# Performance work log

Measured on AMD Instinct MI355X. Metric: run time of the kernel, lower is better.

Reference implementation:

```python
import jax, jax.numpy as jnp
import numpy as np

N = 32000   # nodes
E = 256000  # edges
G = 64      # graphs
IN = 64     # input feature dim
TD = 32     # time embedding dim
D = 128     # hidden dim
HEADS = 4
C = D // HEADS  # per-head channels = 32
ED = 16     # edge feature dim
L = 4       # num SBlocks
FF = 4 * D  # MLP hidden


def _ln(x, g, b):
    m = x.mean(-1, keepdims=True)
    v = ((x - m) ** 2).mean(-1, keepdims=True)
    return (x - m) / jnp.sqrt(v + 1e-5) * g + b


def _time_enc(t):
    half = TD // 2
    fac = jnp.exp(jnp.arange(half, dtype=jnp.float32) * (-jnp.log(10000.0) / (half - 1 + 1e-8)))
    ang = t.astype(jnp.float32)[:, None] * fac[None, :]
    return jnp.concatenate([jnp.sin(ang), jnp.cos(ang)], axis=-1)


def setup_inputs() -> dict:
    key = jax.random.key(0)
    ks = iter(jax.random.split(key, 64))
    nrm = lambda shape: jax.random.normal(next(ks), shape, dtype=jnp.float32) * 0.02
    x = jax.random.normal(next(ks), (N, IN), dtype=jnp.float32)
    t = jax.random.randint(next(ks), (N,), 0, 128, dtype=jnp.int32)
    edge_index = jax.random.randint(next(ks), (2, E), 0, N, dtype=jnp.int32)
    edge_attr = jax.random.normal(next(ks), (E, ED), dtype=jnp.float32)
    batch = jnp.sort(jax.random.randint(next(ks), (N,), 0, G, dtype=jnp.int32))
    p = {
        'Win': nrm((IN + TD, D)), 'b_in': jnp.zeros((D,), jnp.float32),
        'Wq': nrm((L, D, D)), 'bq': jnp.zeros((L, D), jnp.float32),
        'Wk': nrm((L, D, D)), 'bk': jnp.zeros((L, D), jnp.float32),
        'Wv': nrm((L, D, D)), 'bv': jnp.zeros((L, D), jnp.float32),
        'We': nrm((L, ED, D)), 'be': jnp.zeros((L, D), jnp.float32),
        'Wskip': nrm((L, D, D)), 'bskip': jnp.zeros((L, D), jnp.float32),
        'Wbeta': nrm((L, 3 * D)),
        'ln1_g': jnp.ones((L, D), jnp.float32), 'ln1_b': jnp.zeros((L, D), jnp.float32),
        'Wff1': nrm((L, D, FF)), 'bff1': jnp.zeros((L, FF), jnp.float32),
        'Wff2': nrm((L, FF, D)), 'bff2': jnp.zeros((L, D), jnp.float32),
        'ln2_g': jnp.ones((L, D), jnp.float32), 'ln2_b': jnp.zeros((L, D), jnp.float32),
        'Wh1': nrm((2 * D, D)), 'bh1': jnp.zeros((D,), jnp.float32),
        'Wh2': nrm((D, 2)), 'bh2': jnp.zeros((2,), jnp.float32),
    }
    return {'x': x, 't': t, 'edge_index': edge_index, 'edge_attr': edge_attr, 'batch': batch, **p}


def reference(x, t, edge_index, edge_attr, batch, Win, b_in, Wq, bq, Wk, bk, Wv, bv, We, be,
              Wskip, bskip, Wbeta, ln1_g, ln1_b, Wff1, bff1, Wff2, bff2, ln2_g, ln2_b,
              Wh1, bh1, Wh2, bh2):
    # input projection with sinusoidal time encoding
    h = jnp.concatenate([x, _time_enc(t)], axis=-1)
    h = jax.nn.relu(h @ Win + b_in)
    src, dst = edge_index[0], edge_index[1]
    for i in range(L):
        # TransformerConv (multi-head, edge_attr fused into key & value, beta skip)
        q = (h @ Wq[i] + bq[i]).reshape(N, HEADS, C)
        k = (h @ Wk[i] + bk[i]).reshape(N, HEADS, C)
        v = (h @ Wv[i] + bv[i]).reshape(N, HEADS, C)
        e = (edge_attr @ We[i] + be[i]).reshape(E, HEADS, C)
        kj = k[src] + e                     # [E,H,C] gather
        vj = v[src] + e
        alpha = (q[dst] * kj).sum(-1) / jnp.sqrt(jnp.asarray(C, h.dtype))  # [E,H]
        amax = jax.ops.segment_max(alpha, dst, num_segments=N)
        ex = jnp.exp(alpha - amax[dst])
        den = jax.ops.segment_sum(ex, dst, num_segments=N)
        w = ex / den[dst]                   # segment softmax over incoming edges
        out = jax.ops.segment_sum(vj * w[..., None], dst, num_segments=N).reshape(N, D)
        xr = h @ Wskip[i] + bskip[i]
        beta = jax.nn.sigmoid(jnp.concatenate([out, xr, out - xr], -1) @ Wbeta[i])[:, None]
        xs = beta * xr + (1.0 - beta) * out
        h = _ln(h + xs, ln1_g[i], ln1_b[i])
        ff = jax.nn.relu(h @ Wff1[i] + bff1[i]) @ Wff2[i] + bff2[i]
        h = _ln(h + ff, ln2_g[i], ln2_b[i])
    # last-timestep masked readout
    tf = t.astype(h.dtype)
    tmax = jax.ops.segment_max(tf, batch, num_segments=G)
    m = tf == tmax[batch]
    mf = m.astype(h.dtype)[:, None]
    cnt = jax.ops.segment_sum(mf, batch, num_segments=G)
    gmean = jax.ops.segment_sum(h * mf, batch, num_segments=G) / jnp.maximum(cnt, 1.0)
    gmax = jax.ops.segment_max(jnp.where(m[:, None], h, -1e30), batch, num_segments=G)
    g = jnp.concatenate([gmean, gmax], axis=-1)
    return jax.nn.relu(g @ Wh1 + bh1) @ Wh2 + bh2
```

## Files before the change

### kernel.cpp

```cpp
#include <hip/hip_runtime.h>

#define N_NODES 32000
#define N_EDGES 256000
#define N_GRAPH 64
#define NLAYER  4

typedef __attribute__((ext_vector_type(8))) short short8;
typedef __attribute__((ext_vector_type(4))) float f32x4;

__device__ __forceinline__ float bf2f(unsigned short u){
  return __uint_as_float(((unsigned int)u) << 16);
}
__device__ __forceinline__ unsigned short f2bf(float f){
  unsigned int x = __float_as_uint(f);
  x = x + 0x7fffu + ((x >> 16) & 1u);
  return (unsigned short)(x >> 16);
}
__device__ __forceinline__ float ldf(const void* p, int i, int isbf){
  if(isbf) return bf2f(((const unsigned short*)p)[i]);
  return ((const float*)p)[i];
}

__global__ void TactileGAT_43207370997900_kernel() {}

__global__ void sentinel_kernel(unsigned short* out){
  int i = blockIdx.x * 64 + threadIdx.x;
  if(i < 2 * N_GRAPH) out[i] = (unsigned short)0x4000;
}

__global__ void detect_kernel(const unsigned int* ones_words, int* flag){
  if(blockIdx.x == 0 && threadIdx.x == 0)
    flag[0] = (ones_words[0] == 0x3F800000u) ? 0 : 1;
}

__global__ void zero_kernel(int* p, int n){
  int i = blockIdx.x * 256 + threadIdx.x;
  if(i < n) p[i] = 0;
}

__global__ void deg_kernel(const int* dst, int* deg){
  int e = blockIdx.x * 256 + threadIdx.x;
  if(e < N_EDGES) atomicAdd(&deg[dst[e]], 1);
}

__global__ void blocksum_kernel(const int* deg, int* psum){
  __shared__ int s[256];
  int b = blockIdx.x, tid = threadIdx.x;
  int i = b * 256 + tid;
  s[tid] = (i < N_NODES) ? deg[i] : 0;
  __syncthreads();
  for(int off = 128; off > 0; off = off / 2){
    if(tid < off) s[tid] = s[tid] + s[tid + off];
    __syncthreads();
  }
  if(tid == 0) psum[b] = s[0];
}

__global__ void scanp_kernel(int* psum){
  __shared__ int s[128];
  int tid = threadIdx.x;
  int v = (tid < 125) ? psum[tid] : 0;
  s[tid] = v;
  __syncthreads();
  for(int off = 1; off < 128; off = off * 2){
    int tv = (tid >= off) ? s[tid - off] : 0;
    __syncthreads();
    s[tid] = s[tid] + tv;
    __syncthreads();
  }
  if(tid < 125) psum[tid] = s[tid] - v;
}

__global__ void rowptr_kernel(const int* deg, const int* psum, int* rowptr,
                              int* cursor){
  __shared__ int s[256];
  int b = blockIdx.x, tid = threadIdx.x;
  int i = b * 256 + tid;
  int v = (i < N_NODES) ? deg[i] : 0;
  s[tid] = v;
  __syncthreads();
  for(int off = 1; off < 256; off = off * 2){
    int tv = (tid >= off) ? s[tid - off] : 0;
    __syncthreads();
    s[tid] = s[tid] + tv;
    __syncthreads();
  }
  int excl = s[tid] - v + psum[b];
  if(i < N_NODES){ rowptr[i] = excl; cursor[i] = excl; }
  if(i == N_NODES - 1) rowptr[N_NODES] = excl + v;
}

__global__ void scatter_kernel(const int* dst, const int* src, int* cursor,
                               int* csr_e, int* csr_s){
  int e = blockIdx.x * 256 + threadIdx.x;
  if(e < N_EDGES){
    int pos = atomicAdd(&cursor[dst[e]], 1);
    csr_e[pos] = e;
    csr_s[pos] = src[e];
  }
}

__global__ void eap_kernel(const void* ea, const int* csr_e, const int* flag,
                           unsigned short* eap){
  int idx = blockIdx.x * 256 + threadIdx.x;
  if(idx >= N_EDGES * 32) return;
  int slot = idx >> 5, j = idx & 31;
  float v = (j < 16) ? ldf(ea, csr_e[slot] * 16 + j, flag[0]) : 0.f;
  eap[idx] = f2bf(v);
}

__global__ void wep_kernel(const void* We, const int* flag, unsigned short* WeP){
  int idx = blockIdx.x * 256 + threadIdx.x;
  if(idx >= NLAYER * 128 * 32) return;
  int i = idx >> 12, rem = idx & 4095, n = rem >> 5, k = rem & 31;
  float v = (k < 16) ? ldf(We, i * 2048 + k * 128 + n, flag[0]) : 0.f;
  WeP[idx] = f2bf(v);
}

__global__ void pack_kernel(const void* Wq, const void* Wk, const void* Wv,
                            const void* Wsk, const void* Wff1, const void* Wff2,
                            const int* flag, unsigned short* WTq,
                            unsigned short* WT1, unsigned short* WT2){
  int idx = blockIdx.x * 256 + threadIdx.x;
  int isbf = flag[0];
  int i = idx / 196608;
  if(i >= NLAYER) return;
  int rem = idx - i * 196608;
  int seg = rem / 65536;
  int off = rem - seg * 65536;
  if(seg == 0){
    int n = off >> 7, k = off & 127;
    int sel = n >> 7, c = n & 127;
    const void* W = (sel == 0) ? Wq : (sel == 1) ? Wk : (sel == 2) ? Wv : Wsk;
    WTq[i * 65536 + off] = f2bf(ldf(W, i * 16384 + k * 128 + c, isbf));
  } else if(seg == 1){
    int n = off >> 7, k = off & 127;
    WT1[i * 65536 + off] = f2bf(ldf(Wff1, i * 65536 + k * 512 + n, isbf));
  } else {
    int n = off >> 9, k = off & 511;
    WT2[i * 65536 + off] = f2bf(ldf(Wff2, i * 65536 + k * 128 + n, isbf));
  }
}

__global__ void xprep_kernel(const void* x, const int* t, const int* flag,
                             unsigned short* xin){
  int idx = blockIdx.x * 256 + threadIdx.x;
  if(idx >= N_NODES * 128) return;
  int n = idx >> 7, c = idx & 127;
  float v;
  if(c < 64){
    v = ldf(x, n * 64 + c, flag[0]);
  } else if(c < 96){
    int j  = c - 64;
    int jj = (j < 16) ? j : (j - 16);
    float fac = expf((float)jj * (-9.210340371976184f / 15.00000001f));
    float ang = (float)t[n] * fac;
    v = (j < 16) ? sinf(ang) : cosf(ang);
  } else {
    v = 0.f;
  }
  xin[idx] = f2bf(v);
}

__global__ void winp_kernel(const void* Win, const int* flag,
                            unsigned short* WTin){
  int idx = blockIdx.x * 256 + threadIdx.x;
  if(idx >= 128 * 128) return;
  int c = idx >> 7, k = idx & 127;
  float v = (k < 96) ? ldf(Win, k * 128 + c, flag[0]) : 0.f;
  WTin[idx] = f2bf(v);
}

__global__ void gemm_frag(const unsigned short* A, const unsigned short* WT,
                          const void* bias, int boff, const int* flag,
                          int K, int nbx, void* Y, int obf, int ystride,
                          int act){
  int tid = threadIdx.x;
  int bx = blockIdx.x % nbx;
  int by = blockIdx.x / nbx;
  int m0 = by * 128, c0 = bx * 128;
  int wv = tid / 64, lane = tid % 64;
  int q = lane / 16, r = lane % 16;
  const unsigned short* Ap0 = A + (m0 + wv * 32 + r) * K + q * 8;
  const unsigned short* Ap1 = Ap0 + 16 * K;
  const unsigned short* Wp = WT + (c0 + r) * K + q * 8;
  f32x4 acc[2][8];
  for(int g = 0; g < 2; g++)
    for(int tt = 0; tt < 8; tt++)
      for(int i = 0; i < 4; i++) acc[g][tt][i] = 0.f;
  for(int k0 = 0; k0 < K; k0 += 32){
    short8 a0 = *(const short8*)(Ap0 + k0);
    short8 a1 = *(const short8*)(Ap1 + k0);
    for(int tt = 0; tt < 8; tt++){
      short8 b8 = *(const short8*)(Wp + tt * 16 * K + k0);
      acc[0][tt] = __builtin_amdgcn_mfma_f32_16x16x32_bf16(a0, b8, acc[0][tt], 0, 0, 0);
      acc[1][tt] = __builtin_amdgcn_mfma_f32_16x16x32_bf16(a1, b8, acc[1][tt], 0, 0, 0);
    }
  }
  int isbf = flag[0];
  for(int tt = 0; tt < 8; tt++){
    int c = c0 + tt * 16 + r;
    float bv = ldf(bias, boff + c, isbf);
    for(int g = 0; g < 2; g++){
      for(int i = 0; i < 4; i++){
        int row = m0 + wv * 32 + g * 16 + q * 4 + i;
        float v = acc[g][tt][i] + bv;
        if(act == 1) v = fmaxf(v, 0.f);
        if(obf) ((unsigned short*)Y)[row * ystride + c] = f2bf(v);
        else    ((float*)Y)[row * ystride + c] = v;
      }
    }
  }
}

__global__ void edp_frag(const unsigned short* A, const unsigned short* WT,
                         const void* be, int boff, const int* flag,
                         unsigned int* edl){
  int tid = threadIdx.x;
  int m0 = blockIdx.x * 128;
  int wv = tid / 64, lane = tid % 64;
  int q = lane / 16, r = lane % 16;
  const unsigned short* Ap0 = A + (m0 + wv * 32 + r) * 32 + q * 8;
  const unsigned short* Ap1 = Ap0 + 16 * 32;
  const unsigned short* Wp = WT + r * 32 + q * 8;
  f32x4 acc[2][8];
  for(int g = 0; g < 2; g++)
    for(int tt = 0; tt < 8; tt++)
      for(int i = 0; i < 4; i++) acc[g][tt][i] = 0.f;
  short8 a0 = *(const short8*)(Ap0);
  short8 a1 = *(const short8*)(Ap1);
  for(int tt = 0; tt < 8; tt++){
    short8 b8 = *(const short8*)(Wp + tt * 16 * 32);
    acc[0][tt] = __builtin_amdgcn_mfma_f32_16x16x32_bf16(a0, b8, acc[0][tt], 0, 0, 0);
    acc[1][tt] = __builtin_amdgcn_mfma_f32_16x16x32_bf16(a1, b8, acc[1][tt], 0, 0, 0);
  }
  int isbf = flag[0];
  for(int tt = 0; tt < 4; tt++){
    int cc0 = tt * 16 + r;
    float bv0 = ldf(be, boff + cc0, isbf);
    float bv1 = ldf(be, boff + cc0 + 64, isbf);
    for(int g = 0; g < 2; g++){
      for(int i = 0; i < 4; i++){
        int row = m0 + wv * 32 + g * 16 + q * 4 + i;
        unsigned int w = (unsigned int)f2bf(acc[g][tt][i] + bv0)
                       | ((unsigned int)f2bf(acc[g][tt + 4][i] + bv1) << 16);
        edl[(size_t)row * 64 + cc0] = w;
      }
    }
  }
}

__global__ void qkvs_frag(const unsigned short* A, const unsigned short* WTq,
                          const void* b0, const void* b1, const void* b2,
                          const void* b3, int boff, const int* flag,
                          float* qs, unsigned int* kvp){
  int tid = threadIdx.x;
  int sel = blockIdx.x % 4;
  int by  = blockIdx.x / 4;
  int m0 = by * 128;
  int wv = tid / 64, lane = tid % 64;
  int q = lane / 16, r = lane % 16;
  const unsigned short* Ap0 = A + (m0 + wv * 32 + r) * 128 + q * 8;
  const unsigned short* Ap1 = Ap0 + 16 * 128;
  const unsigned short* Wp = WTq + (sel * 128 + r) * 128 + q * 8;
  f32x4 acc[2][8];
  for(int g = 0; g < 2; g++)
    for(int tt = 0; tt < 8; tt++)
      for(int i = 0; i < 4; i++) acc[g][tt][i] = 0.f;
  for(int k0 = 0; k0 < 128; k0 += 32){
    short8 a0 = *(const short8*)(Ap0 + k0);
    short8 a1 = *(const short8*)(Ap1 + k0);
    for(int tt = 0; tt < 8; tt++){
      short8 b8 = *(const short8*)(Wp + tt * 16 * 128 + k0);
      acc[0][tt] = __builtin_amdgcn_mfma_f32_16x16x32_bf16(a0, b8, acc[0][tt], 0, 0, 0);
      acc[1][tt] = __builtin_amdgcn_mfma_f32_16x16x32_bf16(a1, b8, acc[1][tt], 0, 0, 0);
    }
  }
  int isbf = flag[0];
  const void* B = (sel == 0) ? b0 : (sel == 1) ? b1 : (sel == 2) ? b2 : b3;
  if(sel == 0 || sel == 3){
    for(int tt = 0; tt < 8; tt++){
      int cc = tt * 16 + r;
      float bv = ldf(B, boff + cc, isbf);
      for(int g = 0; g < 2; g++){
        for(int i = 0; i < 4; i++){
          int row = m0 + wv * 32 + g * 16 + q * 4 + i;
          float v = acc[g][tt][i] + bv;
          if(sel == 0) qs[row * 256 + cc] = v;
          else         qs[row * 256 + 128 + cc] = v;
        }
      }
    }
  } else {
    int voff = sel - 1;
    for(int tt = 0; tt < 4; tt++){
      int cc0 = tt * 16 + r;
      float bv0 = ldf(B, boff + cc0, isbf);
      float bv1 = ldf(B, boff + cc0 + 64, isbf);
      for(int g = 0; g < 2; g++){
        for(int i = 0; i < 4; i++){
          int row = m0 + wv * 32 + g * 16 + q * 4 + i;
          unsigned int w = (unsigned int)f2bf(acc[g][tt][i] + bv0)
                         | ((unsigned int)f2bf(acc[g][tt + 4][i] + bv1) << 16);
          kvp[row * 128 + 2 * cc0 + voff] = w;
        }
      }
    }
  }
}

#define CH 4
#define ASLICE (CH * 144 + 16)

__device__ __forceinline__ void attn_epilogue(
    int n, int L, float o0, float o1,
    const float* __restrict__ qs, const unsigned short* __restrict__ h,
    const void* Wbeta, int wboff, const void* lng, int lgoff,
    const void* lnb, int lboff, int isbf, unsigned short* __restrict__ h2){
  float xr0 = qs[n * 256 + 128 + L];
  float xr1 = qs[n * 256 + 192 + L];
  float hv0 = bf2f(h[n * 128 + L]);
  float hv1 = bf2f(h[n * 128 + 64 + L]);
  float part = o0 * ldf(Wbeta, wboff + L, isbf)
             + xr0 * ldf(Wbeta, wboff + 128 + L, isbf)
             + (o0 - xr0) * ldf(Wbeta, wboff + 256 + L, isbf)
             + o1 * ldf(Wbeta, wboff + 64 + L, isbf)
             + xr1 * ldf(Wbeta, wboff + 192 + L, isbf)
             + (o1 - xr1) * ldf(Wbeta, wboff + 320 + L, isbf);
#pragma unroll
  for(int mk = 1; mk < 64; mk <<= 1) part += __shfl_xor(part, mk, 64);
  float beta = 1.f / (1.f + __expf(-part));
  float y0 = hv0 + beta * xr0 + (1.f - beta) * o0;
  float y1 = hv1 + beta * xr1 + (1.f - beta) * o1;
  float s = y0 + y1;
#pragma unroll
  for(int mk = 1; mk < 64; mk <<= 1) s += __shfl_xor(s, mk, 64);
  float mean = s * (1.f / 128.f);
  float dy0 = y0 - mean, dy1 = y1 - mean;
  float v2 = dy0 * dy0 + dy1 * dy1;
#pragma unroll
  for(int mk = 1; mk < 64; mk <<= 1) v2 += __shfl_xor(v2, mk, 64);
  float inv = 1.f / sqrtf(v2 * (1.f / 128.f) + 1e-5f);
  h2[n * 128 + L]      = f2bf(dy0 * inv * ldf(lng, lgoff + L, isbf)
                              + ldf(lnb, lboff + L, isbf));
  h2[n * 128 + 64 + L] = f2bf(dy1 * inv * ldf(lng, lgoff + 64 + L, isbf)
                              + ldf(lnb, lboff + 64 + L, isbf));
}

__global__ __launch_bounds__(256, 8)
void attn_epi1_kernel(const float* __restrict__ qs,
                      const unsigned int* __restrict__ kvp,
                      const unsigned int* __restrict__ edl,
                      const int* __restrict__ csr_s,
                      const int* __restrict__ rowptr,
                      const void* __restrict__ Wbeta, int wboff,
                      const void* __restrict__ lng, int lgoff,
                      const void* __restrict__ lnb, int lboff,
                      const unsigned short* __restrict__ h,
                      const int* __restrict__ flag,
                      unsigned short* __restrict__ h2){
  __shared__ float lds[4 * ASLICE];
  int wv = threadIdx.x >> 6, L = threadIdx.x & 63;
  float* sprod  = lds + wv * ASLICE;
  float* salpha = sprod + CH * 144;
  int n = blockIdx.x * 4 + wv;
  int isbf = flag[0];
  int hL = L >> 5, c31 = L & 31;
  float q0 = qs[n * 256 + L]      * 0.17677669529663687f;
  float q1 = qs[n * 256 + 64 + L] * 0.17677669529663687f;
  int beg = rowptr[n], end = rowptr[n + 1];
  float m0 = -1e30f, l0 = 0.f, a0s = 0.f;
  float m1 = -1e30f, l1 = 0.f, a1s = 0.f;
  for(int ci = beg; ci < end; ci += CH){
    int Ep = end - ci; if(Ep > CH) Ep = CH;
    uint2 kw[CH]; unsigned int ew[CH];
#pragma unroll
    for(int i = 0; i < CH; i++){
      kw[i] = make_uint2(0u, 0u); ew[i] = 0u;
      if(i < Ep){
        int s = __builtin_amdgcn_readfirstlane(csr_s[ci + i]);
        kw[i] = *(const uint2*)(kvp + (size_t)s * 128 + 2 * L);
        ew[i] = edl[(size_t)(ci + i) * 64 + L];
      }
    }
    float vd0[CH], vd1[CH];
#pragma unroll
    for(int i = 0; i < CH; i++){
      float e0 = bf2f((unsigned short)(ew[i] & 0xffffu));
      float e1 = bf2f((unsigned short)(ew[i] >> 16));
      float kd0 = bf2f((unsigned short)(kw[i].x & 0xffffu)) + e0;
      float kd1 = bf2f((unsigned short)(kw[i].x >> 16)) + e1;
      vd0[i] = bf2f((unsigned short)(kw[i].y & 0xffffu)) + e0;
      vd1[i] = bf2f((unsigned short)(kw[i].y >> 16)) + e1;
      sprod[i * 144 + hL * 36 + c31]       = q0 * kd0;
      sprod[i * 144 + (2 + hL) * 36 + c31] = q1 * kd1;
    }
    asm volatile("" ::: "memory");
    {
      int i2 = L >> 4, h4 = (L >> 2) & 3, sub = L & 3;
      const f32x4* pp = (const f32x4*)(sprod + i2 * 144 + h4 * 36 + sub * 8);
      f32x4 va = pp[0], vb = pp[1];
      float sv = (va[0] + va[1]) + (va[2] + va[3])
               + ((vb[0] + vb[1]) + (vb[2] + vb[3]));
      sv += __shfl_xor(sv, 1, 64);
      sv += __shfl_xor(sv, 2, 64);
      if(sub == 0) salpha[i2 * 4 + h4] = sv;
    }
    asm volatile("" ::: "memory");
#pragma unroll
    for(int i = 0; i < CH; i++){
      if(i < Ep){
        float p0 = salpha[i * 4 + hL];
        float p1 = salpha[i * 4 + 2 + hL];
        float mn0 = fmaxf(m0, p0), mn1 = fmaxf(m1, p1);
        float g0 = __expf(fminf(p0, m0) - mn0);
        float g1 = __expf(fminf(p1, m1) - mn1);
        float pp0 = (p0 <= m0) ? g0 : 1.f, sc0 = (p0 <= m0) ? 1.f : g0;
        float pp1 = (p1 <= m1) ? g1 : 1.f, sc1 = (p1 <= m1) ? 1.f : g1;
        l0 = l0 * sc0 + pp0;  a0s = a0s * sc0 + pp0 * vd0[i];  m0 = mn0;
        l1 = l1 * sc1 + pp1;  a1s = a1s * sc1 + pp1 * vd1[i];  m1 = mn1;
      }
    }
    asm volatile("" ::: "memory");
  }
  float o0 = (l0 > 0.f) ? a0s / l0 : 0.f;
  float o1 = (l1 > 0.f) ? a1s / l1 : 0.f;
  attn_epilogue(n, L, o0, o1, qs, h, Wbeta, wboff, lng, lgoff, lnb, lboff,
                isbf, h2);
}

__global__ __launch_bounds__(256, 4)
void attn_epi1_inl(const float* __restrict__ qs,
                   const unsigned int* __restrict__ kvp,
                   const unsigned short* __restrict__ eap,
                   const unsigned short* __restrict__ WeP, int lay,
                   const void* __restrict__ be, int beoff,
                   const int* __restrict__ csr_s,
                   const int* __restrict__ rowptr,
                   const void* __restrict__ Wbeta, int wboff,
                   const void* __restrict__ lng, int lgoff,
                   const void* __restrict__ lnb, int lboff,
                   const unsigned short* __restrict__ h,
                   const int* __restrict__ flag,
                   unsigned short* __restrict__ h2){
  __shared__ float lds[4 * ASLICE];
  int wv = threadIdx.x >> 6, L = threadIdx.x & 63;
  float* sprod  = lds + wv * ASLICE;
  float* salpha = sprod + CH * 144;
  int n = blockIdx.x * 4 + wv;
  int isbf = flag[0];
  int hL = L >> 5, c31 = L & 31;
  float wec0[16], wec1[16];
  {
    const short8* wp = (const short8*)(WeP + (size_t)lay * 4096 + L * 32);
    short8 wa = wp[0], wb = wp[1];
    const short8* wq = (const short8*)(WeP + (size_t)lay * 4096 + (L + 64) * 32);
    short8 wc = wq[0], wd = wq[1];
#pragma unroll
    for(int j = 0; j < 8; j++){
      wec0[j]     = bf2f((unsigned short)wa[j]);
      wec0[8 + j] = bf2f((unsigned short)wb[j]);
      wec1[j]     = bf2f((unsigned short)wc[j]);
      wec1[8 + j] = bf2f((unsigned short)wd[j]);
    }
  }
  float be0 = ldf(be, beoff + L, isbf);
  float be1 = ldf(be, beoff + 64 + L, isbf);
  float q0 = qs[n * 256 + L]      * 0.17677669529663687f;
  float q1 = qs[n * 256 + 64 + L] * 0.17677669529663687f;
  int beg = rowptr[n], end = rowptr[n + 1];
  float m0 = -1e30f, l0 = 0.f, a0s = 0.f;
  float m1 = -1e30f, l1 = 0.f, a1s = 0.f;
  for(int ci = beg; ci < end; ci += CH){
    int Ep = end - ci; if(Ep > CH) Ep = CH;
    uint2 kw[CH]; short8 ea_a[CH], ea_b[CH];
#pragma unroll
    for(int i = 0; i < CH; i++){
      kw[i] = make_uint2(0u, 0u);
      ea_a[i] = (short8)0; ea_b[i] = (short8)0;
      if(i < Ep){
        int s = __builtin_amdgcn_readfirstlane(csr_s[ci + i]);
        kw[i] = *(const uint2*)(kvp + (size_t)s * 128 + 2 * L);
        const short8* er = (const short8*)(eap + (size_t)(ci + i) * 32);
        ea_a[i] = er[0]; ea_b[i] = er[1];
      }
    }
    float vd0[CH], vd1[CH];
#pragma unroll
    for(int i = 0; i < CH; i++){
      float ed0 = be0, ed1 = be1;
#pragma unroll
      for(int j = 0; j < 8; j++){
        float va = bf2f((unsigned short)ea_a[i][j]);
        float vb = bf2f((unsigned short)ea_b[i][j]);
        ed0 += va * wec0[j] + vb * wec0[8 + j];
        ed1 += va * wec1[j] + vb * wec1[8 + j];
      }
      float kd0 = bf2f((unsigned short)(kw[i].x & 0xffffu)) + ed0;
      float kd1 = bf2f((unsigned short)(kw[i].x >> 16)) + ed1;
      vd0[i] = bf2f((unsigned short)(kw[i].y & 0xffffu)) + ed0;
      vd1[i] = bf2f((unsigned short)(kw[i].y >> 16)) + ed1;
      sprod[i * 144 + hL * 36 + c31]       = q0 * kd0;
      sprod[i * 144 + (2 + hL) * 36 + c31] = q1 * kd1;
    }
    asm volatile("" ::: "memory");
    {
      int i2 = L >> 4, h4 = (L >> 2) & 3, sub = L & 3;
      const f32x4* pp = (const f32x4*)(sprod + i2 * 144 + h4 * 36 + sub * 8);
      f32x4 va = pp[0], vb = pp[1];
      float sv = (va[0] + va[1]) + (va[2] + va[3])
               + ((vb[0] + vb[1]) + (vb[2] + vb[3]));
      sv += __shfl_xor(sv, 1, 64);
      sv += __shfl_xor(sv, 2, 64);
      if(sub == 0) salpha[i2 * 4 + h4] = sv;
    }
    asm volatile("" ::: "memory");
#pragma unroll
    for(int i = 0; i < CH; i++){
      if(i < Ep){
        float p0 = salpha[i * 4 + hL];
        float p1 = salpha[i * 4 + 2 + hL];
        float mn0 = fmaxf(m0, p0), mn1 = fmaxf(m1, p1);
        float g0 = __expf(fminf(p0, m0) - mn0);
        float g1 = __expf(fminf(p1, m1) - mn1);
        float pp0 = (p0 <= m0) ? g0 : 1.f, sc0 = (p0 <= m0) ? 1.f : g0;
        float pp1 = (p1 <= m1) ? g1 : 1.f, sc1 = (p1 <= m1) ? 1.f : g1;
        l0 = l0 * sc0 + pp0;  a0s = a0s * sc0 + pp0 * vd0[i];  m0 = mn0;
        l1 = l1 * sc1 + pp1;  a1s = a1s * sc1 + pp1 * vd1[i];  m1 = mn1;
      }
    }
    asm volatile("" ::: "memory");
  }
  float o0 = (l0 > 0.f) ? a0s / l0 : 0.f;
  float o1 = (l1 > 0.f) ? a1s / l1 : 0.f;
  attn_epilogue(n, L, o0, o1, qs, h, Wbeta, wboff, lng, lgoff, lnb, lboff,
                isbf, h2);
}

__global__ void ff2_ln_kernel(const unsigned short* A, const unsigned short* WT,
                              const void* bias, int boff,
                              const unsigned short* h2,
                              const void* lng, int lgoff,
                              const void* lnb, int lboff,
                              const int* flag, unsigned short* outh){
  __shared__ float Ys[64 * 133];
  __shared__ float smean[64];
  __shared__ float sinv[64];
  int tid = threadIdx.x;
  int m0 = blockIdx.x * 64;
  int wv = tid / 64, lane = tid % 64;
  int q = lane / 16, r = lane % 16;
  const unsigned short* Ap = A + (m0 + wv * 16 + r) * 512 + q * 8;
  const unsigned short* Wp = WT + r * 512 + q * 8;
  f32x4 acc[8];
  for(int tt = 0; tt < 8; tt++)
    for(int i = 0; i < 4; i++) acc[tt][i] = 0.f;
  for(int k0 = 0; k0 < 512; k0 += 32){
    short8 a8 = *(const short8*)(Ap + k0);
    for(int tt = 0; tt < 8; tt++){
      short8 b8 = *(const short8*)(Wp + tt * 16 * 512 + k0);
      acc[tt] = __builtin_amdgcn_mfma_f32_16x16x32_bf16(a8, b8, acc[tt], 0, 0, 0);
    }
  }
  int isbf = flag[0];
  for(int tt = 0; tt < 8; tt++){
    int c = tt * 16 + r;
    float bv = ldf(bias, boff + c, isbf);
    for(int i = 0; i < 4; i++){
      int rl = wv * 16 + q * 4 + i;
      float v = acc[tt][i] + bv;
      Ys[rl * 133 + c] = bf2f(h2[(m0 + rl) * 128 + c]) + v;
    }
  }
  __syncthreads();
  if(tid < 64){
    float s = 0.f, s2 = 0.f;
    for(int c = 0; c < 128; c++){
      float y = Ys[tid * 133 + c];
      s += y; s2 += y * y;
    }
    float mean = s * (1.f / 128.f);
    float var  = s2 * (1.f / 128.f) - mean * mean;
    smean[tid] = mean;
    sinv[tid]  = 1.f / sqrtf(var + 1e-5f);
  }
  __syncthreads();
  for(int tt = 0; tt < 8; tt++){
    int c = tt * 16 + r;
    float g = ldf(lng, lgoff + c, isbf);
    float b = ldf(lnb, lboff + c, isbf);
    for(int i = 0; i < 4; i++){
      int rl = wv * 16 + q * 4 + i;
      float y = Ys[rl * 133 + c];
      outh[(m0 + rl) * 128 + c] = f2bf((y - smean[rl]) * sinv[rl] * g + b);
    }
  }
}

__global__ void bounds_kernel(const int* batch, int* gstart, int* gend){
  int n = blockIdx.x * 256 + threadIdx.x;
  if(n >= N_NODES) return;
  int b = batch[n];
  if(n == 0 || batch[n - 1] != b) gstart[b] = n;
  if(n == N_NODES - 1 || batch[n + 1] != b) gend[b] = n + 1;
}

__global__ void readout_kernel(const int* t, const unsigned short* h,
                               const int* gstart, const int* gend, float* gbuf){
  __shared__ int redi[128];
  int g = blockIdx.x, d = threadIdx.x;
  int s = gstart[g], e = gend[g];
  int tm = -2147483647;
  for(int nn = s + d; nn < e; nn += 128){
    int tv = t[nn];
    tm = (tv > tm) ? tv : tm;
  }
  redi[d] = tm;
  __syncthreads();
  for(int off = 64; off > 0; off = off / 2){
    if(d < off) redi[d] = (redi[d + off] > redi[d]) ? redi[d + off] : redi[d];
    __syncthreads();
  }
  tm = redi[0];
  float sum = 0.f, mx = -1e30f;
  int cnt = 0;
  for(int nn = s; nn < e; nn++){
    if(t[nn] == tm){
      float hv = bf2f(h[nn * 128 + d]);
      sum += hv;
      mx = fmaxf(mx, hv);
      cnt = cnt + 1;
    }
  }
  gbuf[g * 256 + d]       = sum / (float)((cnt < 1) ? 1 : cnt);
  gbuf[g * 256 + 128 + d] = mx;
}

__global__ void mlp_kernel(const float* gbuf, const void* Wh1, const void* bh1,
                           const void* Wh2, const void* bh2, const int* flag,
                           void* outp){
  __shared__ float gs[256];
  __shared__ float r1[128];
  int g = blockIdx.x, d = threadIdx.x;
  int isbf = flag[0];
  gs[d]       = gbuf[g * 256 + d];
  gs[d + 128] = gbuf[g * 256 + 128 + d];
  __syncthreads();
  float acc = ldf(bh1, d, isbf);
  for(int k = 0; k < 256; k++) acc += gs[k] * ldf(Wh1, k * 128 + d, isbf);
  r1[d] = fmaxf(acc, 0.f);
  __syncthreads();
  if(d < 2){
    float a = ldf(bh2, d, isbf);
    for(int k = 0; k < 128; k++) a += r1[k] * ldf(Wh2, k * 2 + d, isbf);
    if(isbf) ((unsigned short*)outp)[g * 2 + d] = f2bf(a);
    else     ((float*)outp)[g * 2 + d] = a;
  }
}

extern "C" void kernel_launch(void* const* d_in, const int* in_sizes, int n_in,
                              void* d_out, int out_size, void* d_ws, size_t ws_size,
                              hipStream_t stream){
  const void* x          = d_in[0];
  const int*  t          = (const int*)d_in[1];
  const int*  edge_index = (const int*)d_in[2];
  const void* edge_attr  = d_in[3];
  const int*  batch      = (const int*)d_in[4];
  const void* Win  = d_in[5];  const void* b_in = d_in[6];
  const void* Wq   = d_in[7];  const void* bq   = d_in[8];
  const void* Wk   = d_in[9];  const void* bk   = d_in[10];
  const void* Wv   = d_in[11]; const void* bv   = d_in[12];
  const void* We   = d_in[13]; const void* be   = d_in[14];
  const void* Wsk  = d_in[15]; const void* bsk  = d_in[16];
  const void* Wbeta= d_in[17];
  const void* ln1g = d_in[18]; const void* ln1b = d_in[19];
  const void* Wff1 = d_in[20]; const void* bff1 = d_in[21];
  const void* Wff2 = d_in[22]; const void* bff2 = d_in[23];
  const void* ln2g = d_in[24]; const void* ln2b = d_in[25];
  const void* Wh1  = d_in[26]; const void* bh1  = d_in[27];
  const void* Wh2  = d_in[28]; const void* bh2  = d_in[29];
  (void)in_sizes; (void)n_in; (void)out_size;

  char* p = (char*)d_ws;
  unsigned short* h    = (unsigned short*)p; p += (long long)N_NODES * 128 * 2;
  unsigned short* h2   = (unsigned short*)p; p += (long long)N_NODES * 128 * 2;
  float* qs            = (float*)p;          p += (long long)N_NODES * 256 * 4;
  unsigned int* kvp    = (unsigned int*)p;   p += (long long)N_NODES * 128 * 4;
  unsigned short* ffmid= (unsigned short*)p; p += (long long)N_NODES * 512 * 2;
  unsigned short* WTq  = (unsigned short*)p; p += (long long)NLAYER * 65536 * 2;
  unsigned short* WT1  = (unsigned short*)p; p += (long long)NLAYER * 65536 * 2;
  unsigned short* WT2  = (unsigned short*)p; p += (long long)NLAYER * 65536 * 2;
  float* gbuf = (float*)p; p += (long long)N_GRAPH * 256 * 4;
  int* flag   = (int*)p;   p += 4;
  int* rowptr = (int*)p;   p += (long long)(N_NODES + 1) * 4;
  int* cursor = (int*)p;   p += (long long)N_NODES * 4;
  int* deg    = (int*)p;   p += (long long)N_NODES * 4;
  int* gstart = (int*)p;   p += (long long)N_GRAPH * 4;
  int* gend   = (int*)p;   p += (long long)N_GRAPH * 4;
  int* psum   = (int*)p;   p += 128 * 4;
  int* csr_e  = (int*)p;   p += (long long)N_EDGES * 4;
  int* csr_s  = (int*)p;   p += (long long)N_EDGES * 4;
  unsigned short* eap = (unsigned short*)p; p += (long long)N_EDGES * 32 * 2;
  unsigned short* WeP = (unsigned short*)p; p += (long long)NLAYER * 128 * 32 * 2;
  unsigned short* WTin= (unsigned short*)p; p += (long long)128 * 128 * 2;
  unsigned int* edl   = (unsigned int*)p;
  size_t need_edl = (size_t)((char*)edl - (char*)d_ws) + (size_t)N_EDGES * 64 * 4;
  int use_edl = (ws_size >= need_edl) ? 1 : 0;

  unsigned short* xin = ffmid;

  const int* esrc = edge_index;
  const int* edst = edge_index + N_EDGES;

  sentinel_kernel<<<2, 64, 0, stream>>>((unsigned short*)d_out);
  detect_kernel<<<1, 64, 0, stream>>>((const unsigned int*)ln1g, flag);

  int n_zero = N_NODES + 2 * N_GRAPH;
  zero_kernel<<<(n_zero + 255) / 256, 256, 0, stream>>>(deg, n_zero);

  pack_kernel<<<(NLAYER * 196608 + 255) / 256, 256, 0, stream>>>(
      Wq, Wk, Wv, Wsk, Wff1, Wff2, flag, WTq, WT1, WT2);
  deg_kernel<<<N_EDGES / 256, 256, 0, stream>>>(edst, deg);
  blocksum_kernel<<<125, 256, 0, stream>>>(deg, psum);
  scanp_kernel<<<1, 128, 0, stream>>>(psum);
  rowptr_kernel<<<125, 256, 0, stream>>>(deg, psum, rowptr, cursor);
  scatter_kernel<<<N_EDGES / 256, 256, 0, stream>>>(edst, esrc, cursor,
                                                    csr_e, csr_s);
  eap_kernel<<<(N_EDGES * 32) / 256, 256, 0, stream>>>(edge_attr, csr_e, flag, eap);
  wep_kernel<<<(NLAYER * 128 * 32) / 256, 256, 0, stream>>>(We, flag, WeP);

  xprep_kernel<<<(N_NODES * 128) / 256, 256, 0, stream>>>(x, t, flag, xin);
  winp_kernel<<<(128 * 128) / 256, 256, 0, stream>>>(Win, flag, WTin);
  gemm_frag<<<N_NODES / 128, 256, 0, stream>>>(
      xin, WTin, b_in, 0, flag, 128, 1, h, 1, 128, 1);

  int nby = N_NODES / 128;
  for(int i = 0; i < NLAYER; i++){
    if(use_edl)
      edp_frag<<<N_EDGES / 128, 256, 0, stream>>>(
          eap, WeP + (size_t)i * 4096, be, i * 128, flag, edl);
    qkvs_frag<<<4 * nby, 256, 0, stream>>>(
        h, WTq + (long long)i * 65536, bq, bk, bv, bsk, i * 128, flag, qs, kvp);
    if(use_edl)
      attn_epi1_kernel<<<N_NODES / 4, 256, 0, stream>>>(
          qs, kvp, edl, csr_s, rowptr, Wbeta, i * 384,
          ln1g, i * 128, ln1b, i * 128, h, flag, h2);
    else
      attn_epi1_inl<<<N_NODES / 4, 256, 0, stream>>>(
          qs, kvp, eap, WeP, i, be, i * 128, csr_s, rowptr, Wbeta, i * 384,
          ln1g, i * 128, ln1b, i * 128, h, flag, h2);
    gemm_frag<<<4 * nby, 256, 0, stream>>>(
        h2, WT1 + (long long)i * 65536, bff1, i * 512, flag, 128, 4,
        ffmid, 1, 512, 1);
    ff2_ln_kernel<<<N_NODES / 64, 256, 0, stream>>>(
        ffmid, WT2 + (long long)i * 65536, bff2, i * 128, h2,
        ln2g, i * 128, ln2b, i * 128, flag, h);
  }

  bounds_kernel<<<N_NODES / 256, 256, 0, stream>>>(batch, gstart, gend);
  readout_kernel<<<N_GRAPH, 128, 0, stream>>>(t, h, gstart, gend, gbuf);
  mlp_kernel<<<N_GRAPH, 128, 0, stream>>>(gbuf, Wh1, bh1, Wh2, bh2, flag, d_out);
}
```

Measured before the change: 991.3 us.

## Fuse FF1 and FF2+LayerNorm via LDS; widen attention edge chunk to 8

Merges the FF1 GEMM (with ReLU) and the FF2 GEMM + residual + LayerNorm into one kernel. The 512-wide intermediate for 32 rows stays in LDS as bf16, so the global ffmid round trip and one launch per layer go away. Separately, the edge-chunk size in the edl attention kernel goes from 4 to 8 with lower occupancy bounds, giving more loads in flight per chunk. Costs are extra LDS per block (about 33KB) and possibly fewer resident waves, and FF1 weights are reloaded for every 32-row tile.

New measurement: 922.0 us. -7.0%, faster.

```diff
diff --git a/kernel.cpp b/kernel.cpp
--- a/kernel.cpp
+++ b/kernel.cpp
@@ -309,8 +309,8 @@
   }
 }
 
-#define CH 4
-#define ASLICE (CH * 144 + 16)
+#define CH 8
+#define ASLICE (CH * 144 + CH * 4)
 
 __device__ __forceinline__ void attn_epilogue(
     int n, int L, float o0, float o1,
@@ -347,7 +347,7 @@
                               + ldf(lnb, lboff + 64 + L, isbf));
 }
 
-__global__ __launch_bounds__(256, 8)
+__global__ __launch_bounds__(256, 6)
 void attn_epi1_kernel(const float* __restrict__ qs,
                       const unsigned int* __restrict__ kvp,
                       const unsigned int* __restrict__ edl,
@@ -397,14 +397,18 @@
     }
     asm volatile("" ::: "memory");
     {
-      int i2 = L >> 4, h4 = (L >> 2) & 3, sub = L & 3;
-      const f32x4* pp = (const f32x4*)(sprod + i2 * 144 + h4 * 36 + sub * 8);
-      f32x4 va = pp[0], vb = pp[1];
-      float sv = (va[0] + va[1]) + (va[2] + va[3])
-               + ((vb[0] + vb[1]) + (vb[2] + vb[3]));
-      sv += __shfl_xor(sv, 1, 64);
-      sv += __shfl_xor(sv, 2, 64);
-      if(sub == 0) salpha[i2 * 4 + h4] = sv;
+      int i2b = L >> 4, h4 = (L >> 2) & 3, sub = L & 3;
+#pragma unroll
+      for(int half = 0; half < CH / 4; half++){
+        int i2 = i2b + half * 4;
+        const f32x4* pp = (const f32x4*)(sprod + i2 * 144 + h4 * 36 + sub * 8);
+        f32x4 va = pp[0], vb = pp[1];
+        float sv = (va[0] + va[1]) + (va[2] + va[3])
+                 + ((vb[0] + vb[1]) + (vb[2] + vb[3]));
+        sv += __shfl_xor(sv, 1, 64);
+        sv += __shfl_xor(sv, 2, 64);
+        if(sub == 0) salpha[i2 * 4 + h4] = sv;
+      }
     }
     asm volatile("" ::: "memory");
 #pragma unroll
@@ -429,6 +433,8 @@
                 isbf, h2);
 }
 
+#define CH4 4
+#define ASLICE4 (CH4 * 144 + CH4 * 4)
 __global__ __launch_bounds__(256, 4)
 void attn_epi1_inl(const float* __restrict__ qs,
                    const unsigned int* __restrict__ kvp,
@@ -443,10 +449,10 @@
                    const unsigned short* __restrict__ h,
                    const int* __restrict__ flag,
                    unsigned short* __restrict__ h2){
-  __shared__ float lds[4 * ASLICE];
+  __shared__ float lds[4 * ASLICE4];
   int wv = threadIdx.x >> 6, L = threadIdx.x & 63;
-  float* sprod  = lds + wv * ASLICE;
-  float* salpha = sprod + CH * 144;
+  float* sprod  = lds + wv * ASLICE4;
+  float* salpha = sprod + CH4 * 144;
   int n = blockIdx.x * 4 + wv;
   int isbf = flag[0];
   int hL = L >> 5, c31 = L & 31;
@@ -471,11 +477,11 @@
   int beg = rowptr[n], end = rowptr[n + 1];
   float m0 = -1e30f, l0 = 0.f, a0s = 0.f;
   float m1 = -1e30f, l1 = 0.f, a1s = 0.f;
-  for(int ci = beg; ci < end; ci += CH){
-    int Ep = end - ci; if(Ep > CH) Ep = CH;
-    uint2 kw[CH]; short8 ea_a[CH], ea_b[CH];
-#pragma unroll
-    for(int i = 0; i < CH; i++){
+  for(int ci = beg; ci < end; ci += CH4){
+    int Ep = end - ci; if(Ep > CH4) Ep = CH4;
+    uint2 kw[CH4]; short8 ea_a[CH4], ea_b[CH4];
+#pragma unroll
+    for(int i = 0; i < CH4; i++){
       kw[i] = make_uint2(0u, 0u);
       ea_a[i] = (short8)0; ea_b[i] = (short8)0;
       if(i < Ep){
@@ -485,9 +491,9 @@
         ea_a[i] = er[0]; ea_b[i] = er[1];
       }
     }
-    float vd0[CH], vd1[CH];
-#pragma unroll
-    for(int i = 0; i < CH; i++){
+    float vd0[CH4], vd1[CH4];
+#pragma unroll
+    for(int i = 0; i < CH4; i++){
       float ed0 = be0, ed1 = be1;
 #pragma unroll
       for(int j = 0; j < 8; j++){
@@ -516,7 +522,7 @@
     }
     asm volatile("" ::: "memory");
 #pragma unroll
-    for(int i = 0; i < CH; i++){
+    for(int i = 0; i < CH4; i++){
       if(i < Ep){
         float p0 = salpha[i * 4 + hL];
         float p1 = salpha[i * 4 + 2 + hL];
@@ -537,63 +543,108 @@
                 isbf, h2);
 }
 
-__global__ void ff2_ln_kernel(const unsigned short* A, const unsigned short* WT,
-                              const void* bias, int boff,
-                              const unsigned short* h2,
-                              const void* lng, int lgoff,
-                              const void* lnb, int lboff,
-                              const int* flag, unsigned short* outh){
-  __shared__ float Ys[64 * 133];
-  __shared__ float smean[64];
-  __shared__ float sinv[64];
+__global__ __launch_bounds__(256, 4)
+void ff_fused_kernel(const unsigned short* __restrict__ A,
+                     const unsigned short* __restrict__ WT1,
+                     const unsigned short* __restrict__ WT2,
+                     const void* __restrict__ b1, int b1off,
+                     const void* __restrict__ b2, int b2off,
+                     const void* __restrict__ lng, int lgoff,
+                     const void* __restrict__ lnb, int lboff,
+                     const int* __restrict__ flag,
+                     unsigned short* __restrict__ outh){
+  __shared__ __align__(16) float smemf[32 * 520 / 2];
+  __shared__ float smean[32], sinv[32];
+  unsigned short* mid = (unsigned short*)smemf;
+  float* Ys = smemf;
   int tid = threadIdx.x;
-  int m0 = blockIdx.x * 64;
-  int wv = tid / 64, lane = tid % 64;
-  int q = lane / 16, r = lane % 16;
-  const unsigned short* Ap = A + (m0 + wv * 16 + r) * 512 + q * 8;
-  const unsigned short* Wp = WT + r * 512 + q * 8;
-  f32x4 acc[8];
-  for(int tt = 0; tt < 8; tt++)
-    for(int i = 0; i < 4; i++) acc[tt][i] = 0.f;
-  for(int k0 = 0; k0 < 512; k0 += 32){
-    short8 a8 = *(const short8*)(Ap + k0);
+  int m0 = blockIdx.x * 32;
+  int wv = tid >> 6, lane = tid & 63;
+  int q = lane >> 4, r = lane & 15;
+  int isbf = flag[0];
+  {
+    const unsigned short* Ap0 = A + (m0 + r) * 128 + q * 8;
+    const unsigned short* Ap1 = Ap0 + 16 * 128;
+    const unsigned short* Wp = WT1 + (wv * 128 + r) * 128 + q * 8;
+    f32x4 acc[2][8];
+    for(int g = 0; g < 2; g++)
+      for(int tt = 0; tt < 8; tt++)
+        for(int i = 0; i < 4; i++) acc[g][tt][i] = 0.f;
+    for(int k0 = 0; k0 < 128; k0 += 32){
+      short8 a0 = *(const short8*)(Ap0 + k0);
+      short8 a1 = *(const short8*)(Ap1 + k0);
+      for(int tt = 0; tt < 8; tt++){
+        short8 b8 = *(const short8*)(Wp + tt * 16 * 128 + k0);
+        acc[0][tt] = __builtin_amdgcn_mfma_f32_16x16x32_bf16(a0, b8, acc[0][tt], 0, 0, 0);
+        acc[1][tt] = __builtin_amdgcn_mfma_f32_16x16x32_bf16(a1, b8, acc[1][tt], 0, 0, 0);
+      }
+    }
     for(int tt = 0; tt < 8; tt++){
-      short8 b8 = *(const short8*)(Wp + tt * 16 * 512 + k0);
-      acc[tt] = __builtin_amdgcn_mfma_f32_16x16x32_bf16(a8, b8, acc[tt], 0, 0, 0);
-    }
-  }
-  int isbf = flag[0];
-  for(int tt = 0; tt < 8; tt++){
-    int c = tt * 16 + r;
-    float bv = ldf(bias, boff + c, isbf);
-    for(int i = 0; i < 4; i++){
-      int rl = wv * 16 + q * 4 + i;
-      float v = acc[tt][i] + bv;
-      Ys[rl * 133 + c] = bf2f(h2[(m0 + rl) * 128 + c]) + v;
-    }
-  }
-  __syncthreads();
-  if(tid < 64){
+      int c = wv * 128 + tt * 16 + r;
+      float bv = ldf(b1, b1off + c, isbf);
+      for(int g = 0; g < 2; g++){
+        for(int i = 0; i < 4; i++){
+          int row = g * 16 + q * 4 + i;
+          mid[row * 520 + c] = f2bf(fmaxf(acc[g][tt][i] + bv, 0.f));
+        }
+      }
+    }
+  }
+  __syncthreads();
+  f32x4 acc2[2][2];
+  for(int g = 0; g < 2; g++)
+    for(int tt = 0; tt < 2; tt++)
+      for(int i = 0; i < 4; i++) acc2[g][tt][i] = 0.f;
+  {
+    const unsigned short* Wp2 = WT2 + (wv * 32 + r) * 512 + q * 8;
+    for(int k0 = 0; k0 < 512; k0 += 32){
+      short8 a0 = *(const short8*)(mid + r * 520 + k0 + q * 8);
+      short8 a1 = *(const short8*)(mid + (r + 16) * 520 + k0 + q * 8);
+      for(int tt = 0; tt < 2; tt++){
+        short8 b8 = *(const short8*)(Wp2 + tt * 16 * 512 + k0);
+        acc2[0][tt] = __builtin_amdgcn_mfma_f32_16x16x32_bf16(a0, b8, acc2[0][tt], 0, 0, 0);
+        acc2[1][tt] = __builtin_amdgcn_mfma_f32_16x16x32_bf16(a1, b8, acc2[1][tt], 0, 0, 0);
+      }
+    }
+  }
+  __syncthreads();
+  for(int tt = 0; tt < 2; tt++){
+    int c = wv * 32 + tt * 16 + r;
+    float bv = ldf(b2, b2off + c, isbf);
+    for(int g = 0; g < 2; g++){
+      for(int i = 0; i < 4; i++){
+        int row = g * 16 + q * 4 + i;
+        Ys[row * 132 + c] = bf2f(A[(m0 + row) * 128 + c]) + acc2[g][tt][i] + bv;
+      }
+    }
+  }
+  __syncthreads();
+  {
+    int row = tid >> 3, sub = tid & 7;
     float s = 0.f, s2 = 0.f;
-    for(int c = 0; c < 128; c++){
-      float y = Ys[tid * 133 + c];
+    for(int j = 0; j < 16; j++){
+      float y = Ys[row * 132 + sub * 16 + j];
       s += y; s2 += y * y;
     }
-    float mean = s * (1.f / 128.f);
-    float var  = s2 * (1.f / 128.f) - mean * mean;
-    smean[tid] = mean;
-    sinv[tid]  = 1.f / sqrtf(var + 1e-5f);
-  }
-  __syncthreads();
-  for(int tt = 0; tt < 8; tt++){
-    int c = tt * 16 + r;
-    float g = ldf(lng, lgoff + c, isbf);
-    float b = ldf(lnb, lboff + c, isbf);
-    for(int i = 0; i < 4; i++){
-      int rl = wv * 16 + q * 4 + i;
-      float y = Ys[rl * 133 + c];
-      outh[(m0 + rl) * 128 + c] = f2bf((y - smean[rl]) * sinv[rl] * g + b);
-    }
+#pragma unroll
+    for(int mk = 1; mk < 8; mk <<= 1){
+      s  += __shfl_xor(s, mk, 64);
+      s2 += __shfl_xor(s2, mk, 64);
+    }
+    if(sub == 0){
+      float mean = s * (1.f / 128.f);
+      float var  = s2 * (1.f / 128.f) - mean * mean;
+      smean[row] = mean;
+      sinv[row]  = 1.f / sqrtf(var + 1e-5f);
+    }
+  }
+  __syncthreads();
+  for(int tp = 0; tp < 16; tp++){
+    int idx = tp * 256 + tid;
+    int row = idx >> 7, c = idx & 127;
+    float y = Ys[row * 132 + c];
+    outh[(m0 + row) * 128 + c] = f2bf((y - smean[row]) * sinv[row]
+        * ldf(lng, lgoff + c, isbf) + ldf(lnb, lboff + c, isbf));
   }
 }
 
@@ -749,12 +800,9 @@
       attn_epi1_inl<<<N_NODES / 4, 256, 0, stream>>>(
           qs, kvp, eap, WeP, i, be, i * 128, csr_s, rowptr, Wbeta, i * 384,
           ln1g, i * 128, ln1b, i * 128, h, flag, h2);
-    gemm_frag<<<4 * nby, 256, 0, stream>>>(
-        h2, WT1 + (long long)i * 65536, bff1, i * 512, flag, 128, 4,
-        ffmid, 1, 512, 1);
-    ff2_ln_kernel<<<N_NODES / 64, 256, 0, stream>>>(
-        ffmid, WT2 + (long long)i * 65536, bff2, i * 128, h2,
-        ln2g, i * 128, ln2b, i * 128, flag, h);
+    ff_fused_kernel<<<N_NODES / 32, 256, 0, stream>>>(
+        h2, WT1 + (long long)i * 65536, WT2 + (long long)i * 65536,
+        bff1, i * 512, bff2, i * 128, ln2g, i * 128, ln2b, i * 128, flag, h);
   }
 
   bounds_kernel<<<N_NODES / 256, 256, 0, stream>>>(batch, gstart, gend);
```
